# Performance work log

Measured on AMD Instinct MI355X. Metric: run time of the kernel, lower is better.

Reference implementation:

```python
import jax, jax.numpy as jnp
import numpy as np

EMBED_DIM = 1024
NUM_HEADS = 16
HEAD_DIM = EMBED_DIM // NUM_HEADS
B, S = 2, 2048


def setup_inputs() -> dict:
    key = jax.random.key(0)
    k = jax.random.split(key, 8)
    scale = 1.0 / np.sqrt(EMBED_DIM)
    return {
        "x": jax.random.normal(k[0], (B, S, EMBED_DIM), dtype=jnp.float32),
        "x1": jax.random.normal(k[1], (B, S, EMBED_DIM), dtype=jnp.float32),
        "x2": jax.random.normal(k[2], (B, S, EMBED_DIM), dtype=jnp.float32),
        "qkv_w": jax.random.normal(k[3], (3 * EMBED_DIM, EMBED_DIM), dtype=jnp.float32) * scale,
        "qkv_b": jnp.zeros((3 * EMBED_DIM,), dtype=jnp.float32),
        "out_w": jax.random.normal(k[4], (EMBED_DIM, EMBED_DIM), dtype=jnp.float32) * scale,
        "out_b": jnp.zeros((EMBED_DIM,), dtype=jnp.float32),
    }


def reference(x, x1, x2, qkv_w, qkv_b, out_w, out_b):
    # x1, x2 are accepted but unused, matching the torch module.
    b, s, e = x.shape
    qkv = x @ qkv_w.T + qkv_b                      # [B,S,3E]
    qkv = qkv.reshape(b, s, 3, NUM_HEADS, HEAD_DIM)
    qkv = jnp.transpose(qkv, (2, 0, 3, 1, 4))      # [3,B,H,S,D]
    q, k, v = qkv[0], qkv[1], qkv[2]
    scores = jnp.einsum("bhqd,bhkd->bhqk", q, k) / np.sqrt(HEAD_DIM)
    probs = jax.nn.sigmoid(scores)                 # [B,H,S,S]
    sample = jax.random.bernoulli(jax.random.key(42), probs).astype(probs.dtype)
    # straight-through: forward uses sample, gradient flows as identity to probs
    attn = probs + jax.lax.stop_gradient(sample - probs)
    out = jnp.einsum("bhqk,bhkd->bhqd", attn, v)   # [B,H,S,D]
    out = jnp.transpose(out, (0, 2, 1, 3)).reshape(b, s, e)
    return out @ out_w.T + out_b
```

## Files before the change

kernel.cpp:

```cpp
#include <hip/hip_runtime.h>
#include <stdint.h>

#define NB 2
#define NS 2048
#define NE 1024
#define NH 16
#define ND 64

typedef __attribute__((ext_vector_type(8))) short short8;
typedef __attribute__((ext_vector_type(4))) float f4;
typedef __attribute__((ext_vector_type(4))) unsigned short us4;

static __device__ __forceinline__ unsigned short bf16_rne(float x) {
  uint32_t u = __builtin_bit_cast(uint32_t, x);
  u += 0x7fffu + ((u >> 16) & 1u);
  return (unsigned short)(u >> 16);
}
static __device__ __forceinline__ float bf16_f32(unsigned short h) {
  uint32_t u = ((uint32_t)h) << 16;
  return __builtin_bit_cast(float, u);
}

static __device__ __forceinline__ void threefry42(uint32_t x0, uint32_t x1,
                                                  uint32_t& o0, uint32_t& o1) {
  const uint32_t ks0 = 0u, ks1 = 42u;
  const uint32_t ks2 = 0u ^ 42u ^ 0x1BD11BDAu;
  x0 += ks0; x1 += ks1;
#define TF4(a,b,c,d) \
  x0 += x1; x1 = __builtin_rotateleft32(x1, a); x1 ^= x0; \
  x0 += x1; x1 = __builtin_rotateleft32(x1, b); x1 ^= x0; \
  x0 += x1; x1 = __builtin_rotateleft32(x1, c); x1 ^= x0; \
  x0 += x1; x1 = __builtin_rotateleft32(x1, d); x1 ^= x0;
  TF4(13,15,26,6)  x0 += ks1; x1 += ks2 + 1u;
  TF4(17,29,16,24) x0 += ks2; x1 += ks0 + 2u;
  TF4(13,15,26,6)  x0 += ks0; x1 += ks1 + 3u;
  TF4(17,29,16,24) x0 += ks1; x1 += ks2 + 4u;
  TF4(13,15,26,6)  x0 += ks2; x1 += ks0 + 5u;
#undef TF4
  o0 = x0; o1 = x1;
}

static __device__ __forceinline__ void gl2lds16(const void* g, void* l) {
  __builtin_amdgcn_global_load_lds(
      (const __attribute__((address_space(1))) uint32_t*)g,
      (__attribute__((address_space(3))) uint32_t*)l, 16, 0, 0);
}

__global__ void k_split(const float* __restrict__ x, const float* __restrict__ qw,
                        const float* __restrict__ ow,
                        unsigned short* __restrict__ xh, unsigned short* __restrict__ xl,
                        unsigned short* __restrict__ wh, unsigned short* __restrict__ wl,
                        unsigned short* __restrict__ woh) {
  for (uint32_t i = blockIdx.x * 256u + threadIdx.x; i < 8388608u; i += gridDim.x * 256u) {
    if (i < 4194304u) {
      float v = x[i];
      unsigned short hi = bf16_rne(v);
      xh[i] = hi;
      xl[i] = bf16_rne(v - bf16_f32(hi));
    } else if (i < 7340032u) {
      uint32_t j = i - 4194304u;
      float v = qw[j];
      unsigned short hi = bf16_rne(v);
      wh[j] = hi;
      wl[j] = bf16_rne(v - bf16_f32(hi));
    } else {
      uint32_t j = i - 7340032u;
      woh[j] = bf16_rne(ow[j]);
    }
  }
}

__global__ __launch_bounds__(256) void k_qkv(
    const unsigned short* __restrict__ xh, const unsigned short* __restrict__ xl,
    const unsigned short* __restrict__ wh, const unsigned short* __restrict__ wl,
    const float* __restrict__ qkv_b,
    unsigned short* __restrict__ Qh, unsigned short* __restrict__ Ql,
    unsigned short* __restrict__ Kh, unsigned short* __restrict__ Kl,
    unsigned short* __restrict__ Vt) {
  __shared__ unsigned short SM[16384];
  unsigned short* Ah = SM;
  unsigned short* Al = SM + 4096;
  unsigned short* Bh = SM + 8192;
  unsigned short* Bl = SM + 12288;
  const int tid = threadIdx.x;
  const int lane = tid & 63, wid = tid >> 6;
  const int wm = wid >> 1, wn = wid & 1;
  const int bn = blockIdx.x, bm = blockIdx.y;
  const bool isV = (bn >= 16);
  const int quad = lane >> 4, c16 = lane & 15;
  const int ldrow = lane >> 2;
  const int ldk = (lane & 3) * 8;

  f4 acc[4][4];
#pragma unroll
  for (int a = 0; a < 4; ++a)
#pragma unroll
    for (int b = 0; b < 4; ++b) { f4 z = {0.f, 0.f, 0.f, 0.f}; acc[a][b] = z; }

  for (int kt = 0; kt < 32; ++kt) {
    const int k0 = kt * 32;
    __syncthreads();
#pragma unroll
    for (int r = 0; r < 2; ++r) {
      const int c = wid + r * 4;
      const int grow = c * 16 + ldrow;
      const size_t ao = (size_t)(bm * 128 + grow) * 1024 + k0 + ldk;
      const size_t bo = (size_t)(bn * 128 + grow) * 1024 + k0 + ldk;
      const int lo = c * 512 + lane * 8;
      gl2lds16(xh + ao, &Ah[lo]);
      gl2lds16(wh + bo, &Bh[lo]);
      if (!isV) {
        gl2lds16(xl + ao, &Al[lo]);
        gl2lds16(wl + bo, &Bl[lo]);
      }
    }
    __syncthreads();

    short8 ah[4], al[4], bhf[4], blf[4];
#pragma unroll
    for (int t = 0; t < 4; ++t) {
      ah[t] = *(const short8*)&Ah[(wm * 64 + t * 16 + c16) * 32 + quad * 8];
      bhf[t] = *(const short8*)&Bh[(wn * 64 + t * 16 + c16) * 32 + quad * 8];
      if (!isV) {
        al[t] = *(const short8*)&Al[(wm * 64 + t * 16 + c16) * 32 + quad * 8];
        blf[t] = *(const short8*)&Bl[(wn * 64 + t * 16 + c16) * 32 + quad * 8];
      }
    }
    if (isV) {
#pragma unroll
      for (int tm = 0; tm < 4; ++tm)
#pragma unroll
        for (int tn = 0; tn < 4; ++tn)
          acc[tm][tn] = __builtin_amdgcn_mfma_f32_16x16x32_bf16(ah[tm], bhf[tn], acc[tm][tn], 0, 0, 0);
    } else {
#pragma unroll
      for (int tm = 0; tm < 4; ++tm)
#pragma unroll
        for (int tn = 0; tn < 4; ++tn) {
          acc[tm][tn] = __builtin_amdgcn_mfma_f32_16x16x32_bf16(ah[tm], bhf[tn], acc[tm][tn], 0, 0, 0);
          acc[tm][tn] = __builtin_amdgcn_mfma_f32_16x16x32_bf16(ah[tm], blf[tn], acc[tm][tn], 0, 0, 0);
          acc[tm][tn] = __builtin_amdgcn_mfma_f32_16x16x32_bf16(al[tm], bhf[tn], acc[tm][tn], 0, 0, 0);
        }
    }
  }

  if (!isV) {
#pragma unroll
    for (int tm = 0; tm < 4; ++tm) {
#pragma unroll
      for (int tn = 0; tn < 4; ++tn) {
        const int j = bn * 128 + wn * 64 + tn * 16 + c16;
        const float bias = qkv_b[j];
        const int which = j >> 10;
        const int rem = j & 1023;
        const int h = rem >> 6, d = rem & 63;
#pragma unroll
        for (int r = 0; r < 4; ++r) {
          const int i = bm * 128 + wm * 64 + tm * 16 + quad * 4 + r;
          const int b = i >> 11, s = i & 2047;
          const size_t off = (((size_t)(b * 16 + h)) * 2048 + (size_t)s) * 64 + d;
          const float v = acc[tm][tn][r] + bias;
          const unsigned short hi = bf16_rne(v);
          const unsigned short lo = bf16_rne(v - bf16_f32(hi));
          if (which == 0) { Qh[off] = hi; Ql[off] = lo; }
          else            { Kh[off] = hi; Kl[off] = lo; }
        }
      }
    }
  } else {
    __syncthreads();
#pragma unroll
    for (int tm = 0; tm < 4; ++tm) {
#pragma unroll
      for (int tn = 0; tn < 4; ++tn) {
        const int j = bn * 128 + wn * 64 + tn * 16 + c16;
        const float bias = qkv_b[j];
        const int d_local = wn * 64 + tn * 16 + c16;
#pragma unroll
        for (int r = 0; r < 4; ++r) {
          const int s_local = wm * 64 + tm * 16 + quad * 4 + r;
          SM[d_local * 128 + s_local] = bf16_rne(acc[tm][tn][r] + bias);
        }
      }
    }
    __syncthreads();
    const int b = (bm * 128) >> 11;
    const int s0 = (bm * 128) & 2047;
    const int h2 = (bn - 16) * 2;
#pragma unroll
    for (int it = 0; it < 8; ++it) {
      const int chunk = it * 256 + tid;
      const int dr = chunk >> 4;
      const int sc = (chunk & 15) * 8;
      const short8 v = *(const short8*)&SM[dr * 128 + sc];
      const int bh = b * 16 + h2 + (dr >> 6);
      const int d = dr & 63;
      *(short8*)&Vt[((size_t)bh * 64 + d) * 2048 + s0 + sc] = v;
    }
  }
}

__global__ __launch_bounds__(256) void k_attn(
    const unsigned short* __restrict__ Qh, const unsigned short* __restrict__ Ql,
    const unsigned short* __restrict__ Khg, const unsigned short* __restrict__ Klg,
    const unsigned short* __restrict__ Vtg, unsigned short* __restrict__ AO) {
  __shared__ unsigned short Ksh[4096], Ksl[4096], Vs[8192], Pm[4096];
  const int tid = threadIdx.x;
  const int lane = tid & 63, w = tid >> 6;
  const int quad = lane >> 4, c16 = lane & 15;
  const int q0 = blockIdx.x * 64;
  const int bh = blockIdx.y;
  const size_t base = (size_t)bh * (size_t)(2048 * 64);

  const size_t qoff = base + (size_t)(q0 + w * 16 + c16) * 64 + quad * 8;
  const short8 qh0 = *(const short8*)&Qh[qoff];
  const short8 qh1 = *(const short8*)&Qh[qoff + 32];
  const short8 ql0 = *(const short8*)&Ql[qoff];
  const short8 ql1 = *(const short8*)&Ql[qoff + 32];

  const uint32_t fb = (uint32_t)bh * 4194304u +
                      (uint32_t)(q0 + w * 16 + quad * 4) * 2048u + (uint32_t)c16;

  const int c0 = tid, r0 = c0 >> 3, g0 = ((c0 & 7) - r0) & 7;
  const int c1 = tid + 256, r1 = c1 >> 3, g1 = ((c1 & 7) - r1) & 7;

  f4 oacc[4];
#pragma unroll
  for (int s = 0; s < 4; ++s) { f4 z = {0.f, 0.f, 0.f, 0.f}; oacc[s] = z; }

  auto stage = [&](int kb, int vbuf) {
    const size_t koff = base + (size_t)kb * 64;
    gl2lds16(Khg + koff + r0 * 64 + g0 * 8, &Ksh[c0 * 8]);
    gl2lds16(Klg + koff + r0 * 64 + g0 * 8, &Ksl[c0 * 8]);
    gl2lds16(Vtg + base + (size_t)r0 * 2048 + kb + g0 * 8, &Vs[vbuf * 4096 + c0 * 8]);
    gl2lds16(Khg + koff + r1 * 64 + g1 * 8, &Ksh[c1 * 8]);
    gl2lds16(Klg + koff + r1 * 64 + g1 * 8, &Ksl[c1 * 8]);
    gl2lds16(Vtg + base + (size_t)r1 * 2048 + kb + g1 * 8, &Vs[vbuf * 4096 + c1 * 8]);
  };

  stage(0, 0);

  for (int kt = 0; kt < 32; ++kt) {
    const int kb = kt * 64;
    const int vb = (kt & 1) * 4096;
    __syncthreads();

    f4 sacc[4];
#pragma unroll
    for (int sub = 0; sub < 4; ++sub) {
      const int rK = sub * 16 + c16;
      const int sA = ((quad + rK) & 7) * 8;
      const int sB = ((quad + 4 + rK) & 7) * 8;
      const short8 kh0 = *(const short8*)&Ksh[rK * 64 + sA];
      const short8 kh1 = *(const short8*)&Ksh[rK * 64 + sB];
      const short8 kl0 = *(const short8*)&Ksl[rK * 64 + sA];
      const short8 kl1 = *(const short8*)&Ksl[rK * 64 + sB];
      f4 s = {0.f, 0.f, 0.f, 0.f};
      s = __builtin_amdgcn_mfma_f32_16x16x32_bf16(qh0, kh0, s, 0, 0, 0);
      s = __builtin_amdgcn_mfma_f32_16x16x32_bf16(qh1, kh1, s, 0, 0, 0);
      s = __builtin_amdgcn_mfma_f32_16x16x32_bf16(qh0, kl0, s, 0, 0, 0);
      s = __builtin_amdgcn_mfma_f32_16x16x32_bf16(qh1, kl1, s, 0, 0, 0);
      s = __builtin_amdgcn_mfma_f32_16x16x32_bf16(ql0, kh0, s, 0, 0, 0);
      s = __builtin_amdgcn_mfma_f32_16x16x32_bf16(ql1, kh1, s, 0, 0, 0);
      sacc[sub] = s;
    }
    __syncthreads();
    if (kt < 31) stage(kb + 64, (kt & 1) ^ 1);

#pragma unroll
    for (int sub = 0; sub < 4; ++sub) {
      const int qP = sub * 2 + (c16 >> 3);
#pragma unroll
      for (int rr = 0; rr < 4; ++rr) {
        const uint32_t f = fb + (uint32_t)(rr * 2048) + (uint32_t)(kb + sub * 16);
        uint32_t o0, o1;
        threefry42(0u, f, o0, o1);
        const float m = (float)((o0 ^ o1) >> 9);
        const float e = __builtin_amdgcn_exp2f(sacc[sub][rr] * -0.18033688f);
        const int rP = w * 16 + quad * 4 + rr;
        const int addr = rP * 64 + (((qP + rP) & 7) * 8) + (c16 & 7);
        Pm[addr] = (fmaf(m, e, m) < 8388608.0f) ? 0x3F80u : 0u;
      }
    }

    const int rp = w * 16 + c16;
    const short8 pa0 = *(const short8*)&Pm[rp * 64 + ((quad + rp) & 7) * 8];
    const short8 pa1 = *(const short8*)&Pm[rp * 64 + ((quad + 4 + rp) & 7) * 8];
#pragma unroll
    for (int sub = 0; sub < 4; ++sub) {
      const int rV = sub * 16 + c16;
      const short8 vv0 = *(const short8*)&Vs[vb + rV * 64 + ((quad + rV) & 7) * 8];
      const short8 vv1 = *(const short8*)&Vs[vb + rV * 64 + ((quad + 4 + rV) & 7) * 8];
      oacc[sub] = __builtin_amdgcn_mfma_f32_16x16x32_bf16(pa0, vv0, oacc[sub], 0, 0, 0);
      oacc[sub] = __builtin_amdgcn_mfma_f32_16x16x32_bf16(pa1, vv1, oacc[sub], 0, 0, 0);
    }
  }

  const int b = bh >> 4, hh = bh & 15;
#pragma unroll
  for (int sub = 0; sub < 4; ++sub)
#pragma unroll
    for (int r = 0; r < 4; ++r) {
      const int srow = b * 2048 + q0 + w * 16 + quad * 4 + r;
      AO[(size_t)srow * 1024 + hh * 64 + sub * 16 + c16] = bf16_rne(oacc[sub][r]);
    }
}

__global__ __launch_bounds__(256) void k_out(
    const unsigned short* __restrict__ A, const unsigned short* __restrict__ Bw,
    const float* __restrict__ out_b, float* __restrict__ out) {
  __shared__ unsigned short As[128 * 32], Bs[128 * 32];
  const int tid = threadIdx.x;
  const int lane = tid & 63, wid = tid >> 6;
  const int wm = wid >> 1, wn = wid & 1;
  const int bn = blockIdx.x, bm = blockIdx.y;
  const int quad = lane >> 4, c16 = lane & 15;
  const int ldrow = lane >> 2;
  const int ldk = (lane & 3) * 8;

  f4 acc[4][4];
#pragma unroll
  for (int a = 0; a < 4; ++a)
#pragma unroll
    for (int b = 0; b < 4; ++b) { f4 z = {0.f, 0.f, 0.f, 0.f}; acc[a][b] = z; }

  for (int kt = 0; kt < 32; ++kt) {
    const int k0 = kt * 32;
    __syncthreads();
#pragma unroll
    for (int r = 0; r < 2; ++r) {
      const int c = wid + r * 4;
      const int grow = c * 16 + ldrow;
      const size_t ao = (size_t)(bm * 128 + grow) * 1024 + k0 + ldk;
      const size_t bo = (size_t)(bn * 128 + grow) * 1024 + k0 + ldk;
      const int lo = c * 512 + lane * 8;
      gl2lds16(A + ao, &As[lo]);
      gl2lds16(Bw + bo, &Bs[lo]);
    }
    __syncthreads();

    short8 af[4], bf[4];
#pragma unroll
    for (int t = 0; t < 4; ++t) {
      af[t] = *(const short8*)&As[(wm * 64 + t * 16 + c16) * 32 + quad * 8];
      bf[t] = *(const short8*)&Bs[(wn * 64 + t * 16 + c16) * 32 + quad * 8];
    }
#pragma unroll
    for (int tm = 0; tm < 4; ++tm)
#pragma unroll
      for (int tn = 0; tn < 4; ++tn)
        acc[tm][tn] = __builtin_amdgcn_mfma_f32_16x16x32_bf16(af[tm], bf[tn], acc[tm][tn], 0, 0, 0);
  }

#pragma unroll
  for (int tm = 0; tm < 4; ++tm) {
#pragma unroll
    for (int tn = 0; tn < 4; ++tn) {
      const int j = bn * 128 + wn * 64 + tn * 16 + c16;
      const float bias = out_b[j];
#pragma unroll
      for (int r = 0; r < 4; ++r) {
        const int i = bm * 128 + wm * 64 + tm * 16 + quad * 4 + r;
        out[(size_t)i * 1024 + j] = acc[tm][tn][r] + bias;
      }
    }
  }
}

extern "C" void kernel_launch(void* const* d_in, const int* in_sizes, int n_in,
                              void* d_out, int out_size, void* d_ws, size_t ws_size,
                              hipStream_t stream) {
  const float* x     = (const float*)d_in[0];
  const float* qkv_w = (const float*)d_in[3];
  const float* qkv_b = (const float*)d_in[4];
  const float* out_w = (const float*)d_in[5];
  const float* out_b = (const float*)d_in[6];
  float* out = (float*)d_out;

  unsigned short* xh  = (unsigned short*)d_ws;
  unsigned short* xl  = xh + 4194304;
  unsigned short* wh  = xl + 4194304;
  unsigned short* wl  = wh + 3145728;
  unsigned short* woh = wl + 3145728;
  unsigned short* Vt  = woh + 1048576;
  unsigned short* Qh  = Vt + 4194304;
  unsigned short* Ql  = Qh + 4194304;
  unsigned short* Kh  = Ql + 4194304;
  unsigned short* Kl  = Kh + 4194304;
  unsigned short* AO  = xh;

  k_split<<<8192, 256, 0, stream>>>(x, qkv_w, out_w, xh, xl, wh, wl, woh);
  k_qkv<<<dim3(24, 32), 256, 0, stream>>>(xh, xl, wh, wl, qkv_b, Qh, Ql, Kh, Kl, Vt);
  k_attn<<<dim3(32, 32), 256, 0, stream>>>(Qh, Ql, Kh, Kl, Vt, AO);
  k_out<<<dim3(8, 32), 256, 0, stream>>>(AO, woh, out_b, out);
}
```

Measured before the change: 508.4 us.

## Split attention over key halves with 512-thread blocks and byte mask

The attention kernel now uses 512-thread blocks covering 128 queries each and splits the key range into two halves along a new grid z dimension. Each half writes its own bf16 partial output, and the output projection sums the two partials while loading its A tile. The probability mask in shared memory is stored as bytes and expanded to bf16 in registers. The aim is more parallelism and less LDS traffic per tile. In exchange, the partial outputs are rounded to bf16 twice, which adds error, and k_out does extra global reads and conversion work in its load path.

```diff
diff --git a/kernel.cpp b/kernel.cpp
--- a/kernel.cpp
+++ b/kernel.cpp
@@ -200,17 +200,21 @@
   }
 }
 
-__global__ __launch_bounds__(256) void k_attn(
+__global__ __launch_bounds__(512, 8) void k_attn(
     const unsigned short* __restrict__ Qh, const unsigned short* __restrict__ Ql,
     const unsigned short* __restrict__ Khg, const unsigned short* __restrict__ Klg,
     const unsigned short* __restrict__ Vtg, unsigned short* __restrict__ AO) {
-  __shared__ unsigned short Ksh[4096], Ksl[4096], Vs[8192], Pm[4096];
+  __shared__ unsigned short Ksh[4096], Ksl[4096], Vs[8192];
+  __shared__ unsigned char Pmb[8192];
   const int tid = threadIdx.x;
   const int lane = tid & 63, w = tid >> 6;
   const int quad = lane >> 4, c16 = lane & 15;
-  const int q0 = blockIdx.x * 64;
+  const int q0 = blockIdx.x * 128;
   const int bh = blockIdx.y;
+  const int ks = blockIdx.z;
+  const int kbase = ks * 1024;
   const size_t base = (size_t)bh * (size_t)(2048 * 64);
+  unsigned short* AOp = AO + (size_t)ks * 4194304u;
 
   const size_t qoff = base + (size_t)(q0 + w * 16 + c16) * 64 + quad * 8;
   const short8 qh0 = *(const short8*)&Qh[qoff];
@@ -221,8 +225,7 @@
   const uint32_t fb = (uint32_t)bh * 4194304u +
                       (uint32_t)(q0 + w * 16 + quad * 4) * 2048u + (uint32_t)c16;
 
-  const int c0 = tid, r0 = c0 >> 3, g0 = ((c0 & 7) - r0) & 7;
-  const int c1 = tid + 256, r1 = c1 >> 3, g1 = ((c1 & 7) - r1) & 7;
+  const int r0 = tid >> 3, g0 = ((tid & 7) - r0) & 7;
 
   f4 oacc[4];
 #pragma unroll
@@ -230,18 +233,15 @@
 
   auto stage = [&](int kb, int vbuf) {
     const size_t koff = base + (size_t)kb * 64;
-    gl2lds16(Khg + koff + r0 * 64 + g0 * 8, &Ksh[c0 * 8]);
-    gl2lds16(Klg + koff + r0 * 64 + g0 * 8, &Ksl[c0 * 8]);
-    gl2lds16(Vtg + base + (size_t)r0 * 2048 + kb + g0 * 8, &Vs[vbuf * 4096 + c0 * 8]);
-    gl2lds16(Khg + koff + r1 * 64 + g1 * 8, &Ksh[c1 * 8]);
-    gl2lds16(Klg + koff + r1 * 64 + g1 * 8, &Ksl[c1 * 8]);
-    gl2lds16(Vtg + base + (size_t)r1 * 2048 + kb + g1 * 8, &Vs[vbuf * 4096 + c1 * 8]);
+    gl2lds16(Khg + koff + r0 * 64 + g0 * 8, &Ksh[tid * 8]);
+    gl2lds16(Klg + koff + r0 * 64 + g0 * 8, &Ksl[tid * 8]);
+    gl2lds16(Vtg + base + (size_t)r0 * 2048 + kb + g0 * 8, &Vs[vbuf * 4096 + tid * 8]);
   };
 
-  stage(0, 0);
-
-  for (int kt = 0; kt < 32; ++kt) {
-    const int kb = kt * 64;
+  stage(kbase, 0);
+
+  for (int kt = 0; kt < 16; ++kt) {
+    const int kb = kbase + kt * 64;
     const int vb = (kt & 1) * 4096;
     __syncthreads();
 
@@ -265,11 +265,10 @@
       sacc[sub] = s;
     }
     __syncthreads();
-    if (kt < 31) stage(kb + 64, (kt & 1) ^ 1);
+    if (kt < 15) stage(kb + 64, (kt & 1) ^ 1);
 
 #pragma unroll
     for (int sub = 0; sub < 4; ++sub) {
-      const int qP = sub * 2 + (c16 >> 3);
 #pragma unroll
       for (int rr = 0; rr < 4; ++rr) {
         const uint32_t f = fb + (uint32_t)(rr * 2048) + (uint32_t)(kb + sub * 16);
@@ -277,15 +276,24 @@
         threefry42(0u, f, o0, o1);
         const float m = (float)((o0 ^ o1) >> 9);
         const float e = __builtin_amdgcn_exp2f(sacc[sub][rr] * -0.18033688f);
-        const int rP = w * 16 + quad * 4 + rr;
-        const int addr = rP * 64 + (((qP + rP) & 7) * 8) + (c16 & 7);
-        Pm[addr] = (fmaf(m, e, m) < 8388608.0f) ? 0x3F80u : 0u;
+        const int row = w * 16 + quad * 4 + rr;
+        Pmb[row * 64 + sub * 16 + c16] = (fmaf(m, e, m) < 8388608.0f) ? 0x40u : 0u;
       }
     }
 
     const int rp = w * 16 + c16;
-    const short8 pa0 = *(const short8*)&Pm[rp * 64 + ((quad + rp) & 7) * 8];
-    const short8 pa1 = *(const short8*)&Pm[rp * 64 + ((quad + 4 + rp) & 7) * 8];
+    const uint32_t plo0 = *(const uint32_t*)&Pmb[rp * 64 + quad * 8];
+    const uint32_t phi0 = *(const uint32_t*)&Pmb[rp * 64 + quad * 8 + 4];
+    const uint32_t plo1 = *(const uint32_t*)&Pmb[rp * 64 + 32 + quad * 8];
+    const uint32_t phi1 = *(const uint32_t*)&Pmb[rp * 64 + 32 + quad * 8 + 4];
+    short8 pa0, pa1;
+#pragma unroll
+    for (int j = 0; j < 4; ++j) {
+      pa0[j]     = (plo0 & (0x40u << (8 * j))) ? (short)0x3F80 : (short)0;
+      pa0[j + 4] = (phi0 & (0x40u << (8 * j))) ? (short)0x3F80 : (short)0;
+      pa1[j]     = (plo1 & (0x40u << (8 * j))) ? (short)0x3F80 : (short)0;
+      pa1[j + 4] = (phi1 & (0x40u << (8 * j))) ? (short)0x3F80 : (short)0;
+    }
 #pragma unroll
     for (int sub = 0; sub < 4; ++sub) {
       const int rV = sub * 16 + c16;
@@ -302,12 +310,13 @@
 #pragma unroll
     for (int r = 0; r < 4; ++r) {
       const int srow = b * 2048 + q0 + w * 16 + quad * 4 + r;
-      AO[(size_t)srow * 1024 + hh * 64 + sub * 16 + c16] = bf16_rne(oacc[sub][r]);
+      AOp[(size_t)srow * 1024 + hh * 64 + sub * 16 + c16] = bf16_rne(oacc[sub][r]);
     }
 }
 
 __global__ __launch_bounds__(256) void k_out(
-    const unsigned short* __restrict__ A, const unsigned short* __restrict__ Bw,
+    const unsigned short* __restrict__ A0, const unsigned short* __restrict__ A1,
+    const unsigned short* __restrict__ Bw,
     const float* __restrict__ out_b, float* __restrict__ out) {
   __shared__ unsigned short As[128 * 32], Bs[128 * 32];
   const int tid = threadIdx.x;
@@ -334,7 +343,14 @@
       const size_t ao = (size_t)(bm * 128 + grow) * 1024 + k0 + ldk;
       const size_t bo = (size_t)(bn * 128 + grow) * 1024 + k0 + ldk;
       const int lo = c * 512 + lane * 8;
-      gl2lds16(A + ao, &As[lo]);
+      const short8 a0 = *(const short8*)&A0[ao];
+      const short8 a1 = *(const short8*)&A1[ao];
+      short8 acm;
+#pragma unroll
+      for (int j = 0; j < 8; ++j)
+        acm[j] = (short)bf16_rne(bf16_f32((unsigned short)a0[j]) +
+                                 bf16_f32((unsigned short)a1[j]));
+      *(short8*)&As[lo] = acm;
       gl2lds16(Bw + bo, &Bs[lo]);
     }
     __syncthreads();
@@ -387,10 +403,11 @@
   unsigned short* Ql  = Qh + 4194304;
   unsigned short* Kh  = Ql + 4194304;
   unsigned short* Kl  = Kh + 4194304;
-  unsigned short* AO  = xh;
+  unsigned short* AO0 = xh;
+  unsigned short* AO1 = xl;
 
   k_split<<<8192, 256, 0, stream>>>(x, qkv_w, out_w, xh, xl, wh, wl, woh);
   k_qkv<<<dim3(24, 32), 256, 0, stream>>>(xh, xl, wh, wl, qkv_b, Qh, Ql, Kh, Kl, Vt);
-  k_attn<<<dim3(32, 32), 256, 0, stream>>>(Qh, Ql, Kh, Kl, Vt, AO);
-  k_out<<<dim3(8, 32), 256, 0, stream>>>(AO, woh, out_b, out);
-}
+  k_attn<<<dim3(16, 32, 2), 512, 0, stream>>>(Qh, Ql, Kh, Kl, Vt, AO0);
+  k_out<<<dim3(8, 32), 256, 0, stream>>>(AO0, AO1, woh, out_b, out);
+}
```

New measurement: 562.1 us. +10.6%, slower.
